# Optimization experiments

Measured on AMD Instinct MI355X. Metric: run time of the kernel, lower is better.

The kernel has to match this reference:

```python
import jax, jax.numpy as jnp
import numpy as np

N = 100000
E = 3200000
F_IN = 128
H1, H2 = 32, 16
R = 8
G = 512  # number of graphs in batch


def setup_inputs() -> dict:
    key = jax.random.key(0)
    ks = jax.random.split(key, 12)
    x = jax.random.normal(ks[0], (N, F_IN), dtype=jnp.float32)
    edge_index = jax.random.randint(ks[1], (2, E), 0, N, dtype=jnp.int64)
    edge_attr = jax.random.randint(ks[2], (E,), 0, R, dtype=jnp.int64)
    batch = jnp.sort(jax.random.randint(ks[3], (N,), 0, G, dtype=jnp.int64))
    s1 = 1.0 / np.sqrt(F_IN)
    s2 = 1.0 / np.sqrt(H1)
    s3 = 1.0 / np.sqrt(H2)
    W1 = jax.random.uniform(ks[4], (R, F_IN, H1), jnp.float32, -s1, s1)
    root1 = jax.random.uniform(ks[5], (F_IN, H1), jnp.float32, -s1, s1)
    b1 = jnp.zeros((H1,), jnp.float32)
    W2 = jax.random.uniform(ks[6], (R, H1, H2), jnp.float32, -s2, s2)
    root2 = jax.random.uniform(ks[7], (H1, H2), jnp.float32, -s2, s2)
    b2 = jnp.zeros((H2,), jnp.float32)
    dense_w = jax.random.uniform(ks[8], (H2, 1), jnp.float32, -s3, s3)
    dense_b = jax.random.uniform(ks[9], (1,), jnp.float32, -s3, s3)
    return dict(x=x, edge_index=edge_index, edge_attr=edge_attr, batch=batch,
                W1=W1, root1=root1, b1=b1, W2=W2, root2=root2, b2=b2,
                dense_w=dense_w, dense_b=dense_b)


def rgcn_layer(x, W, root, b, src, dst, rel, num_rel):
    # Per-relation transform of all nodes: [N, R, out]
    xw = jnp.einsum('ni,rio->nro', x, W)
    msgs = xw[src, rel]                      # gather per edge: [E, out]
    seg = dst * num_rel + rel                # (node, relation) segment id
    nr = x.shape[0] * num_rel
    sums = jax.ops.segment_sum(msgs, seg, num_segments=nr)
    cnt = jax.ops.segment_sum(jnp.ones(src.shape, x.dtype), seg, num_segments=nr)
    mean = sums / jnp.maximum(cnt, 1.0)[:, None]
    agg = mean.reshape(x.shape[0], num_rel, -1).sum(axis=1)  # sum over relations
    return agg + x @ root + b


def reference(x, edge_index, edge_attr, batch, W1, root1, b1, W2, root2, b2, dense_w, dense_b):
    src, dst = edge_index[0], edge_index[1]
    rel = edge_attr
    h = jax.nn.relu(rgcn_layer(x, W1, root1, b1, src, dst, rel, R))
    # F.dropout is treated as identity (inference) for a deterministic reference
    h = jax.nn.relu(rgcn_layer(h, W2, root2, b2, src, dst, rel, R))
    pooled = jax.ops.segment_max(h, batch, num_segments=G)
    pooled = jnp.where(jnp.isfinite(pooled), pooled, 0.0)  # empty graphs -> 0
    return pooled @ dense_w + dense_b
```

## Files before the change

### kernel.cpp

```cpp
#include <hip/hip_runtime.h>
#include <hip/hip_bf16.h>

#define RNUM 8
#define HH1 32
#define HH2 16
#define FIN 128
#define BNODES 256
#define NBMAX 512
#define PCHUNK 8192
#define SORTCAP 11264

#define W1STR 136
#define W1ELTS (288 * W1STR)
#define W2STR 40
#define W2ELTS (144 * W2STR)

typedef short bf16x8 __attribute__((ext_vector_type(8)));
typedef float f32x4 __attribute__((ext_vector_type(4)));

__device__ inline bf16x8 cvt8(const float* __restrict__ p) {
  float tmp[8];
  *(float4*)tmp = *(const float4*)p;
  *(float4*)(tmp + 4) = *(const float4*)(p + 4);
  bf16x8 r;
  #pragma unroll
  for (int j = 0; j < 8; ++j) {
    union { __hip_bfloat16 h; short s; } cv;
    cv.h = __float2bfloat16(tmp[j]);
    r[j] = cv.s;
  }
  return r;
}

__device__ inline bf16x8 cvt8relu(const float* __restrict__ p) {
  float tmp[8];
  *(float4*)tmp = *(const float4*)p;
  *(float4*)(tmp + 4) = *(const float4*)(p + 4);
  bf16x8 r;
  #pragma unroll
  for (int j = 0; j < 8; ++j) {
    union { __hip_bfloat16 h; short s; } cv;
    cv.h = __float2bfloat16(fmaxf(tmp[j], 0.f));
    r[j] = cv.s;
  }
  return r;
}

__global__ __launch_bounds__(256) void k_bhist(const int* __restrict__ ei,
    int* __restrict__ ghist, int E, int NB) {
  __shared__ int h[NBMAX];
  int t = threadIdx.x;
  for (int i = t; i < NBMAX; i += 256) h[i] = 0;
  __syncthreads();
  int base = blockIdx.x * 4096;
  #pragma unroll
  for (int j = 0; j < 16; ++j) {
    int e = base + j * 256 + t;
    if (e < E) atomicAdd(&h[ei[E + e] >> 8], 1);
  }
  __syncthreads();
  for (int i = t; i < NB; i += 256)
    if (h[i]) atomicAdd(&ghist[i], h[i]);
}

__global__ __launch_bounds__(NBMAX) void k_bscan(const int* __restrict__ ghist,
    int* __restrict__ bbase, int* __restrict__ gcursor, int NB, int E) {
  __shared__ int buf[NBMAX];
  int t = threadIdx.x;
  int v = (t < NB) ? ghist[t] : 0;
  buf[t] = v;
  __syncthreads();
  for (int d = 1; d < NBMAX; d <<= 1) {
    int w = (t >= d) ? buf[t - d] : 0;
    __syncthreads();
    buf[t] += w;
    __syncthreads();
  }
  if (t < NB) {
    int ex = buf[t] - v;
    bbase[t] = ex;
    gcursor[t] = ex;
  }
  if (t == 0) bbase[NB] = E;
}

__global__ __launch_bounds__(512) void k_part(const int* __restrict__ ei,
    const int* __restrict__ ea, int* __restrict__ gcursor,
    unsigned* __restrict__ ebuf, int E, int NB) {
  __shared__ unsigned reorder[PCHUNK];
  __shared__ unsigned short bkt[PCHUNK];
  __shared__ int hist[NBMAX], startl[NBMAX], cursor[NBMAX], gb[NBMAX], scanb[NBMAX];
  int t = threadIdx.x;
  int base = blockIdx.x * PCHUNK;
  int cn = min(PCHUNK, E - base);
  unsigned key[16];
  short bb[16];
  hist[t] = 0;
  __syncthreads();
  #pragma unroll
  for (int j = 0; j < 16; ++j) {
    int e = base + j * 512 + t;
    bb[j] = -1;
    if (e < E) {
      int src = ei[e], dst = ei[E + e], rel = ea[e];
      key[j] = ((unsigned)(dst & (BNODES - 1)) << 20) | ((unsigned)src << 3) | (unsigned)rel;
      int b = dst >> 8;
      bb[j] = (short)b;
      atomicAdd(&hist[b], 1);
    }
  }
  __syncthreads();
  int v = hist[t];
  scanb[t] = v;
  __syncthreads();
  for (int d = 1; d < NBMAX; d <<= 1) {
    int w = (t >= d) ? scanb[t - d] : 0;
    __syncthreads();
    scanb[t] += w;
    __syncthreads();
  }
  startl[t] = scanb[t] - v;
  cursor[t] = scanb[t] - v;
  __syncthreads();
  #pragma unroll
  for (int j = 0; j < 16; ++j) {
    if (bb[j] >= 0) {
      int pos = atomicAdd(&cursor[bb[j]], 1);
      reorder[pos] = key[j];
      bkt[pos] = (unsigned short)bb[j];
    }
  }
  __syncthreads();
  if (t < NB && hist[t] > 0) gb[t] = atomicAdd(&gcursor[t], hist[t]);
  __syncthreads();
  for (int p = t; p < cn; p += 512) {
    int b = bkt[p];
    ebuf[gb[b] + (p - startl[b])] = reorder[p];
  }
}

__global__ __launch_bounds__(512) void k_sort(const int* __restrict__ bbase,
    const unsigned* __restrict__ ebuf, unsigned* __restrict__ ebuf2,
    float* __restrict__ wbuf, int* __restrict__ rps, int* __restrict__ rpc,
    int NB) {
  __shared__ int hist[2048];
  __shared__ float invw[2048];
  __shared__ int dlc[256];
  __shared__ unsigned sorted[SORTCAP];
  int t = threadIdx.x;
  int b = blockIdx.x;
  int s = bbase[b], e = bbase[b + 1];
  int out_s = ((s + 7) & ~7) + (b << 11);
  for (int i = t; i < 2048; i += 512) hist[i] = 0;
  __syncthreads();
  for (int p = s + t; p < e; p += 512) {
    unsigned k = ebuf[p];
    atomicAdd(&hist[((k >> 20) << 3) | (k & 7u)], 1);
  }
  __syncthreads();
  for (int i = t; i < 2048; i += 512) {
    int c = hist[i];
    invw[i] = 1.0f / (float)(c > 1 ? c : 1);
  }
  __syncthreads();
  int pr[8];
  int cdl = 0, pc = 0;
  if (t < 256) {
    #pragma unroll
    for (int r = 0; r < 8; ++r) { pr[r] = cdl; cdl += hist[8 * t + r]; }
    pc = (cdl + 7) & ~7;
    dlc[t] = pc;
  }
  __syncthreads();
  for (int d = 1; d < 256; d <<= 1) {
    int w = (t < 256 && t >= d) ? dlc[t - d] : 0;
    __syncthreads();
    if (t < 256) dlc[t] += w;
    __syncthreads();
  }
  if (t < 256) {
    int ebase = dlc[t] - pc;
    #pragma unroll
    for (int r = 0; r < 8; ++r) hist[8 * t + r] = ebase + pr[r];
    rps[(b << 8) + t] = out_s + ebase;
    rpc[(b << 8) + t] = cdl;
  }
  __syncthreads();
  int ptot = dlc[255];
  if (ptot <= SORTCAP) {
    for (int p = t; p < ptot; p += 512) sorted[p] = 0xFFFFFFFFu;
    __syncthreads();
    for (int p = s + t; p < e; p += 512) {
      unsigned k = ebuf[p];
      int pos = atomicAdd(&hist[((k >> 20) << 3) | (k & 7u)], 1);
      sorted[pos] = k;
    }
    __syncthreads();
    for (int p = t; p < ptot; p += 512) {
      unsigned k = sorted[p];
      int o = out_s + p;
      if (k == 0xFFFFFFFFu) { ebuf2[o] = 0u; wbuf[o] = 0.f; }
      else { ebuf2[o] = k; wbuf[o] = invw[((k >> 20) << 3) | (k & 7u)]; }
    }
  } else {
    if (t < 256) {
      int ebase = dlc[t] - pc;
      for (int p = ebase + cdl; p < dlc[t]; ++p) {
        ebuf2[out_s + p] = 0u; wbuf[out_s + p] = 0.f;
      }
    }
    __syncthreads();
    for (int p = s + t; p < e; p += 512) {
      unsigned k = ebuf[p];
      int bin = ((k >> 20) << 3) | (k & 7u);
      int pos = atomicAdd(&hist[bin], 1);
      ebuf2[out_s + pos] = k;
      wbuf[out_s + pos] = invw[bin];
    }
  }
}

__global__ __launch_bounds__(256) void k_prepw(const float* __restrict__ W1,
    const float* __restrict__ root1, const float* __restrict__ W2,
    const float* __restrict__ root2, unsigned short* __restrict__ Wcat,
    unsigned short* __restrict__ W2cat) {
  int id = blockIdx.x * 256 + threadIdx.x;
  union { __hip_bfloat16 h; unsigned short u; } cv;
  if (id < W1ELTS) {
    int c = id / W1STR, kk = id - c * W1STR;
    float v = 0.f;
    if (kk < FIN)
      v = (c < 256) ? W1[((size_t)(c >> 5) * FIN + kk) * HH1 + (c & 31)]
                    : root1[(size_t)kk * HH1 + (c - 256)];
    cv.h = __float2bfloat16(v);
    Wcat[id] = cv.u;
  } else if (id < W1ELTS + W2ELTS) {
    int id2 = id - W1ELTS;
    int c = id2 / W2STR, kk = id2 - c * W2STR;
    float v = 0.f;
    if (kk < HH1)
      v = (c < 128) ? W2[((size_t)(c >> 4) * HH1 + kk) * HH2 + (c & 15)]
                    : root2[(size_t)kk * HH2 + (c - 128)];
    cv.h = __float2bfloat16(v);
    W2cat[id2] = cv.u;
  }
}

__global__ __launch_bounds__(256) void k_gemm1m(const float* __restrict__ x,
    const unsigned short* __restrict__ Wcat, const float* __restrict__ b1,
    __hip_bfloat16* __restrict__ xw, float* __restrict__ agg, int N) {
  __shared__ short WL[W1ELTS];
  int t = threadIdx.x;
  for (int i = t; i < W1ELTS / 8; i += 256)
    ((uint4*)WL)[i] = ((const uint4*)Wcat)[i];
  __syncthreads();
  int lane = t & 63;
  int wv = t >> 6;
  int g = lane >> 4, lc = lane & 15;
  long nb = (long)blockIdx.x * 128 + wv * 32;
  f32x4 acc[2][18];
  #pragma unroll
  for (int m = 0; m < 2; ++m)
    #pragma unroll
    for (int j = 0; j < 18; ++j)
      acc[m][j] = (f32x4){0.f, 0.f, 0.f, 0.f};
  long rowA0 = nb + lc;       if (rowA0 > N - 1) rowA0 = N - 1;
  long rowA1 = nb + 16 + lc;  if (rowA1 > N - 1) rowA1 = N - 1;
  #pragma unroll
  for (int ks = 0; ks < 4; ++ks) {
    int ko = ks * 32 + g * 8;
    bf16x8 a0 = cvt8(x + rowA0 * FIN + ko);
    bf16x8 a1 = cvt8(x + rowA1 * FIN + ko);
    #pragma unroll
    for (int j = 0; j < 18; ++j) {
      bf16x8 bf = *(const bf16x8*)(WL + (16 * j + lc) * W1STR + ko);
      acc[0][j] = __builtin_amdgcn_mfma_f32_16x16x32_bf16(a0, bf, acc[0][j], 0, 0, 0);
      acc[1][j] = __builtin_amdgcn_mfma_f32_16x16x32_bf16(a1, bf, acc[1][j], 0, 0, 0);
    }
  }
  #pragma unroll
  for (int m = 0; m < 2; ++m) {
    #pragma unroll
    for (int j = 0; j < 18; ++j) {
      #pragma unroll
      for (int q = 0; q < 4; ++q) {
        long row = nb + 16 * m + g * 4 + q;
        if (row < N) {
          if (j < 16) {
            xw[row * 256 + 16 * j + lc] = __float2bfloat16(acc[m][j][q]);
          } else {
            int cc = (j - 16) * 16 + lc;
            agg[row * HH1 + cc] = acc[m][j][q] + b1[cc];
          }
        }
      }
    }
  }
}

__global__ __launch_bounds__(256) void k_agg1(const int* __restrict__ rps,
    const int* __restrict__ rpc, const unsigned* __restrict__ eb,
    const float* __restrict__ wb, const __hip_bfloat16* __restrict__ xw,
    float* __restrict__ agg, int N) {
  int d = blockIdx.x * 4 + (threadIdx.x >> 6);
  if (d >= N) return;
  int lane = threadIdx.x & 63;
  int h = lane & 31, half = lane >> 5;
  int s = rps[d];
  int cnt = rpc[d];
  float acc = 0.f;
  for (int j = half * 8; j < cnt; j += 16) {
    const unsigned* kp = eb + s + j;
    uint4 ka = *(const uint4*)kp;
    uint4 kb = *(const uint4*)(kp + 4);
    float4 wa = *(const float4*)(wb + s + j);
    float4 wc = *(const float4*)(wb + s + j + 4);
    unsigned ks[8] = {ka.x, ka.y, ka.z, ka.w, kb.x, kb.y, kb.z, kb.w};
    float ws[8] = {wa.x, wa.y, wa.z, wa.w, wc.x, wc.y, wc.z, wc.w};
    #pragma unroll
    for (int u = 0; u < 8; ++u) {
      unsigned idx = ks[u] & 0xFFFFFu;
      float v = __bfloat162float(xw[((size_t)idx << 5) + h]);
      acc = fmaf(ws[u], v, acc);
    }
  }
  acc += __shfl_xor(acc, 32);
  if (half == 0) agg[((size_t)d << 5) + h] += acc;
}

__global__ __launch_bounds__(256) void k_gemm2m(const float* __restrict__ agg1,
    const unsigned short* __restrict__ W2cat, const float* __restrict__ b2,
    __hip_bfloat16* __restrict__ xw, float* __restrict__ agg, int N) {
  __shared__ short WL[W2ELTS];
  int t = threadIdx.x;
  for (int i = t; i < W2ELTS / 8; i += 256)
    ((uint4*)WL)[i] = ((const uint4*)W2cat)[i];
  __syncthreads();
  int lane = t & 63;
  int wv = t >> 6;
  int g = lane >> 4, lc = lane & 15;
  long nb = (long)blockIdx.x * 128 + wv * 32;
  f32x4 acc[2][9];
  #pragma unroll
  for (int m = 0; m < 2; ++m)
    #pragma unroll
    for (int j = 0; j < 9; ++j)
      acc[m][j] = (f32x4){0.f, 0.f, 0.f, 0.f};
  long rowA0 = nb + lc;       if (rowA0 > N - 1) rowA0 = N - 1;
  long rowA1 = nb + 16 + lc;  if (rowA1 > N - 1) rowA1 = N - 1;
  bf16x8 a0 = cvt8relu(agg1 + rowA0 * HH1 + g * 8);
  bf16x8 a1 = cvt8relu(agg1 + rowA1 * HH1 + g * 8);
  #pragma unroll
  for (int j = 0; j < 9; ++j) {
    bf16x8 bf = *(const bf16x8*)(WL + (16 * j + lc) * W2STR + g * 8);
    acc[0][j] = __builtin_amdgcn_mfma_f32_16x16x32_bf16(a0, bf, acc[0][j], 0, 0, 0);
    acc[1][j] = __builtin_amdgcn_mfma_f32_16x16x32_bf16(a1, bf, acc[1][j], 0, 0, 0);
  }
  #pragma unroll
  for (int m = 0; m < 2; ++m) {
    #pragma unroll
    for (int j = 0; j < 9; ++j) {
      #pragma unroll
      for (int q = 0; q < 4; ++q) {
        long row = nb + 16 * m + g * 4 + q;
        if (row < N) {
          if (j < 8) {
            xw[row * 128 + 16 * j + lc] = __float2bfloat16(acc[m][j][q]);
          } else {
            agg[row * HH2 + lc] = acc[m][j][q] + b2[lc];
          }
        }
      }
    }
  }
}

__global__ __launch_bounds__(256) void k_agg2(const int* __restrict__ rps,
    const int* __restrict__ rpc, const unsigned* __restrict__ eb,
    const float* __restrict__ wb, const __hip_bfloat16* __restrict__ xw,
    float* __restrict__ agg, int N) {
  int d = blockIdx.x * 4 + (threadIdx.x >> 6);
  if (d >= N) return;
  int lane = threadIdx.x & 63;
  int h = lane & 15, q = lane >> 4;
  int s = rps[d];
  int cnt = rpc[d];
  float acc = 0.f;
  for (int j = q * 8; j < cnt; j += 32) {
    const unsigned* kp = eb + s + j;
    uint4 ka = *(const uint4*)kp;
    uint4 kb = *(const uint4*)(kp + 4);
    float4 wa = *(const float4*)(wb + s + j);
    float4 wc = *(const float4*)(wb + s + j + 4);
    unsigned ks[8] = {ka.x, ka.y, ka.z, ka.w, kb.x, kb.y, kb.z, kb.w};
    float ws[8] = {wa.x, wa.y, wa.z, wa.w, wc.x, wc.y, wc.z, wc.w};
    #pragma unroll
    for (int u = 0; u < 8; ++u) {
      unsigned idx = ks[u] & 0xFFFFFu;
      float v = __bfloat162float(xw[((size_t)idx << 4) + h]);
      acc = fmaf(ws[u], v, acc);
    }
  }
  acc += __shfl_xor(acc, 32);
  acc += __shfl_xor(acc, 16);
  if (q == 0) agg[((size_t)d << 4) + h] += acc;
}

__global__ __launch_bounds__(256) void k_pool(const float* __restrict__ agg2,
    const int* __restrict__ batch, unsigned* __restrict__ pooled, int N) {
  int gid = blockIdx.x * 256 + threadIdx.x;
  int n = gid >> 4;
  if (n < N) {
    int h = gid & 15;
    float v = fmaxf(agg2[(size_t)n * HH2 + h], 0.f);
    atomicMax(&pooled[batch[n] * HH2 + h], __float_as_uint(v));
  }
}

__global__ __launch_bounds__(256) void k_dense(const float* __restrict__ pooled,
    const float* __restrict__ dw, const float* __restrict__ db,
    float* __restrict__ out, int Gn) {
  int g = blockIdx.x * 256 + threadIdx.x;
  if (g < Gn) {
    float s = db[0];
    #pragma unroll
    for (int h = 0; h < HH2; ++h) s += pooled[(size_t)g * HH2 + h] * dw[h];
    out[g] = s;
  }
}

extern "C" void kernel_launch(void* const* d_in, const int* in_sizes, int n_in,
                              void* d_out, int out_size, void* d_ws, size_t ws_size,
                              hipStream_t stream) {
  const float* x     = (const float*)d_in[0];
  const int*   ei    = (const int*)d_in[1];
  const int*   ea    = (const int*)d_in[2];
  const int*   batch = (const int*)d_in[3];
  const float* W1    = (const float*)d_in[4];
  const float* root1 = (const float*)d_in[5];
  const float* b1    = (const float*)d_in[6];
  const float* W2    = (const float*)d_in[7];
  const float* root2 = (const float*)d_in[8];
  const float* b2    = (const float*)d_in[9];
  const float* dw    = (const float*)d_in[10];
  const float* db    = (const float*)d_in[11];
  float* out = (float*)d_out;

  const int N  = in_sizes[0] / FIN;
  const int E  = in_sizes[2];
  const int Gn = out_size;
  const int NB = (N + BNODES - 1) / BNODES;

  char* ws = (char*)d_ws;
  size_t off = 0;
  auto walloc = [&](size_t bytes) -> void* {
    void* p = (void*)(ws + off);
    off += (bytes + 255) & ~(size_t)255;
    return p;
  };
  const size_t EP = (size_t)E + (size_t)NBMAX * 2048 + 64;
  int*            ghist   = (int*)            walloc((size_t)NBMAX * 4);
  int*            bbase   = (int*)            walloc(((size_t)NBMAX + 1) * 4);
  int*            gcursor = (int*)            walloc((size_t)NBMAX * 4);
  unsigned*       ebuf    = (unsigned*)       walloc((size_t)E * 4);
  unsigned*       ebuf2   = (unsigned*)       walloc(EP * 4);
  float*          wbuf    = (float*)          walloc(EP * 4);
  int*            rps     = (int*)            walloc((size_t)NBMAX * 256 * 4);
  int*            rpc     = (int*)            walloc((size_t)NBMAX * 256 * 4);
  unsigned short* Wcat    = (unsigned short*) walloc((size_t)W1ELTS * 2);
  unsigned short* W2cat   = (unsigned short*) walloc((size_t)W2ELTS * 2);
  __hip_bfloat16* xw1     = (__hip_bfloat16*) walloc((size_t)N * RNUM * HH1 * 2);
  float*          agg1    = (float*)          walloc((size_t)N * HH1 * 4);
  __hip_bfloat16* xw2     = (__hip_bfloat16*) walloc((size_t)N * RNUM * HH2 * 2);
  float*          agg2    = (float*)          walloc((size_t)N * HH2 * 4);
  unsigned*       pooled  = (unsigned*)       walloc((size_t)Gn * HH2 * 4);

  hipMemsetAsync(ghist, 0, (size_t)NBMAX * 4, stream);
  hipMemsetAsync(pooled, 0, (size_t)Gn * HH2 * 4, stream);

  k_prepw<<<(W1ELTS + W2ELTS + 255) / 256, 256, 0, stream>>>(W1, root1, W2, root2, Wcat, W2cat);
  k_bhist<<<(E + 4095) / 4096, 256, 0, stream>>>(ei, ghist, E, NB);
  k_bscan<<<1, NBMAX, 0, stream>>>(ghist, bbase, gcursor, NB, E);
  k_part<<<(E + PCHUNK - 1) / PCHUNK, 512, 0, stream>>>(ei, ea, gcursor, ebuf, E, NB);
  k_sort<<<NB, 512, 0, stream>>>(bbase, ebuf, ebuf2, wbuf, rps, rpc, NB);

  k_gemm1m<<<(N + 127) / 128, 256, 0, stream>>>(x, Wcat, b1, xw1, agg1, N);
  k_agg1<<<(N + 3) / 4, 256, 0, stream>>>(rps, rpc, ebuf2, wbuf, xw1, agg1, N);
  k_gemm2m<<<(N + 127) / 128, 256, 0, stream>>>(agg1, W2cat, b2, xw2, agg2, N);
  k_agg2<<<(N + 3) / 4, 256, 0, stream>>>(rps, rpc, ebuf2, wbuf, xw2, agg2, N);
  k_pool<<<(int)(((long)N * HH2 + 255) / 256), 256, 0, stream>>>(agg2, batch, pooled, N);
  k_dense<<<(Gn + 255) / 256, 256, 0, stream>>>((const float*)pooled, dw, db, out, Gn);
}
```

Before: 286.4 us.

## Split layer-1 GEMM columns across waves with register-resident weights, drop LDS staging

Reworks the first-layer GEMM so each of 6 waves owns 3 column tiles (48 of the 288 output columns) and keeps its weight fragments in registers, loaded straight from global memory. The per-block LDS copy of the 78KB weight matrix and its barrier are removed. Each block now processes two 64-row tiles. The aim is to cut the LDS fill cost and LDS pressure so more blocks fit per CU. In exchange, every wave reloads and converts the same x rows from global memory, and x traffic is now duplicated six-fold within a block.

```diff
diff --git a/kernel.cpp b/kernel.cpp
--- a/kernel.cpp
+++ b/kernel.cpp
@@ -246,51 +246,58 @@
   }
 }
 
-__global__ __launch_bounds__(256) void k_gemm1m(const float* __restrict__ x,
+__global__ __launch_bounds__(384) void k_gemm1m(const float* __restrict__ x,
     const unsigned short* __restrict__ Wcat, const float* __restrict__ b1,
     __hip_bfloat16* __restrict__ xw, float* __restrict__ agg, int N) {
-  __shared__ short WL[W1ELTS];
-  int t = threadIdx.x;
-  for (int i = t; i < W1ELTS / 8; i += 256)
-    ((uint4*)WL)[i] = ((const uint4*)Wcat)[i];
-  __syncthreads();
-  int lane = t & 63;
-  int wv = t >> 6;
+  int lane = threadIdx.x & 63;
+  int wv = threadIdx.x >> 6;
   int g = lane >> 4, lc = lane & 15;
-  long nb = (long)blockIdx.x * 128 + wv * 32;
-  f32x4 acc[2][18];
-  #pragma unroll
-  for (int m = 0; m < 2; ++m)
-    #pragma unroll
-    for (int j = 0; j < 18; ++j)
-      acc[m][j] = (f32x4){0.f, 0.f, 0.f, 0.f};
-  long rowA0 = nb + lc;       if (rowA0 > N - 1) rowA0 = N - 1;
-  long rowA1 = nb + 16 + lc;  if (rowA1 > N - 1) rowA1 = N - 1;
-  #pragma unroll
-  for (int ks = 0; ks < 4; ++ks) {
-    int ko = ks * 32 + g * 8;
-    bf16x8 a0 = cvt8(x + rowA0 * FIN + ko);
-    bf16x8 a1 = cvt8(x + rowA1 * FIN + ko);
-    #pragma unroll
-    for (int j = 0; j < 18; ++j) {
-      bf16x8 bf = *(const bf16x8*)(WL + (16 * j + lc) * W1STR + ko);
-      acc[0][j] = __builtin_amdgcn_mfma_f32_16x16x32_bf16(a0, bf, acc[0][j], 0, 0, 0);
-      acc[1][j] = __builtin_amdgcn_mfma_f32_16x16x32_bf16(a1, bf, acc[1][j], 0, 0, 0);
-    }
-  }
-  #pragma unroll
-  for (int m = 0; m < 2; ++m) {
-    #pragma unroll
-    for (int j = 0; j < 18; ++j) {
+  int cj0 = wv * 3;
+  bf16x8 B[3][4];
+  #pragma unroll
+  for (int j = 0; j < 3; ++j)
+    #pragma unroll
+    for (int ks = 0; ks < 4; ++ks)
+      B[j][ks] = *(const bf16x8*)(Wcat + (size_t)((cj0 + j) * 16 + lc) * W1STR + ks * 32 + g * 8);
+
+  #pragma unroll
+  for (int tt = 0; tt < 2; ++tt) {
+    long base = ((long)blockIdx.x * 2 + tt) * 64;
+    if (base >= N) break;
+    f32x4 acc[4][3];
+    #pragma unroll
+    for (int rf = 0; rf < 4; ++rf)
       #pragma unroll
-      for (int q = 0; q < 4; ++q) {
-        long row = nb + 16 * m + g * 4 + q;
-        if (row < N) {
-          if (j < 16) {
-            xw[row * 256 + 16 * j + lc] = __float2bfloat16(acc[m][j][q]);
-          } else {
-            int cc = (j - 16) * 16 + lc;
-            agg[row * HH1 + cc] = acc[m][j][q] + b1[cc];
+      for (int j = 0; j < 3; ++j)
+        acc[rf][j] = (f32x4){0.f, 0.f, 0.f, 0.f};
+    #pragma unroll
+    for (int rf = 0; rf < 4; ++rf) {
+      long row = base + rf * 16 + lc;
+      if (row > N - 1) row = N - 1;
+      bf16x8 a[4];
+      #pragma unroll
+      for (int ks = 0; ks < 4; ++ks)
+        a[ks] = cvt8(x + row * FIN + ks * 32 + g * 8);
+      #pragma unroll
+      for (int j = 0; j < 3; ++j)
+        #pragma unroll
+        for (int ks = 0; ks < 4; ++ks)
+          acc[rf][j] = __builtin_amdgcn_mfma_f32_16x16x32_bf16(a[ks], B[j][ks], acc[rf][j], 0, 0, 0);
+    }
+    #pragma unroll
+    for (int rf = 0; rf < 4; ++rf) {
+      #pragma unroll
+      for (int j = 0; j < 3; ++j) {
+        int col = (cj0 + j) * 16 + lc;
+        #pragma unroll
+        for (int q = 0; q < 4; ++q) {
+          long row = base + rf * 16 + g * 4 + q;
+          if (row < N) {
+            if (col < 256) {
+              xw[row * 256 + col] = __float2bfloat16(acc[rf][j][q]);
+            } else {
+              agg[row * HH1 + (col - 256)] = acc[rf][j][q] + b1[col - 256];
+            }
           }
         }
       }
@@ -484,7 +491,7 @@
   k_part<<<(E + PCHUNK - 1) / PCHUNK, 512, 0, stream>>>(ei, ea, gcursor, ebuf, E, NB);
   k_sort<<<NB, 512, 0, stream>>>(bbase, ebuf, ebuf2, wbuf, rps, rpc, NB);
 
-  k_gemm1m<<<(N + 127) / 128, 256, 0, stream>>>(x, Wcat, b1, xw1, agg1, N);
+  k_gemm1m<<<(N + 127) / 128, 384, 0, stream>>>(x, Wcat, b1, xw1, agg1, N);
   k_agg1<<<(N + 3) / 4, 256, 0, stream>>>(rps, rpc, ebuf2, wbuf, xw1, agg1, N);
   k_gemm2m<<<(N + 127) / 128, 256, 0, stream>>>(agg1, W2cat, b2, xw2, agg2, N);
   k_agg2<<<(N + 3) / 4, 256, 0, stream>>>(rps, rpc, ebuf2, wbuf, xw2, agg2, N);
```

After: 318.6 us. 11.2% more time.
